# Optimization experiments

Measured on AMD Instinct MI355X. Metric: run time of the kernel, lower is better.

## Reference

```python
import jax, jax.numpy as jnp
import numpy as np

N = 16777216  # batch*A*width*height (flat anchor-score vector)
BINS = 10
LOSS_WEIGHT = 1.0


def setup_inputs() -> dict:
    key = jax.random.key(0)
    k1, k2, k3 = jax.random.split(key, 3)
    pred = jax.random.normal(k1, (N,), dtype=jnp.float32)          # IoU logits
    target = jax.random.uniform(k2, (N,), dtype=jnp.float32)       # IoU targets in [0,1]
    label_weight = (jax.random.uniform(k3, (N,)) > 0.3).astype(jnp.float32)  # 1=valid, 0=ignore
    return {"pred": pred, "target": target, "label_weight": label_weight, "bins": BINS}


def reference(pred, target, label_weight, bins):
    # target is detached in the original module
    target = jax.lax.stop_gradient(target)
    # gradient norm g = |sigmoid(pred).detach() - target|, lies in [0,1]
    g = jnp.abs(jax.lax.stop_gradient(jax.nn.sigmoid(pred)) - target)
    valid = label_weight > 0
    validf = valid.astype(jnp.float32)
    tot = jnp.maximum(jnp.sum(validf), 1.0)

    # edges are i/bins with last edge nudged by 1e-6, so bin = floor(g*bins) clipped to bins-1
    bin_idx = jnp.clip((g * bins).astype(jnp.int32), 0, bins - 1)
    counts = jax.ops.segment_sum(validf, bin_idx, num_segments=bins)  # per-bin valid counts
    n = jnp.sum(counts > 0).astype(jnp.float32)                        # number of nonempty bins
    counts_safe = jnp.maximum(counts, 1.0)
    w_per_bin = jnp.where(counts > 0, tot / counts_safe, 0.0) / jnp.maximum(n, 1.0)
    weights = jnp.where(valid, w_per_bin[bin_idx], 0.0)

    # weighted BCE-with-logits, reduction='sum', stable form: logaddexp(0,x) - x*z
    bce = jnp.logaddexp(0.0, pred) - pred * target
    loss = jnp.sum(weights * bce) / tot
    return loss * LOSS_WEIGHT
```

## Files before the change

### kernel.cpp

```cpp
#include <hip/hip_runtime.h>

#define BINS 10
#define REPLICAS 16
#define NBLOCKS 2048
#define NTHREADS 256


typedef float vfloat4 __attribute__((ext_vector_type(4)));

__global__ __launch_bounds__(NTHREADS, 4)
void ghm_pass1(const float* __restrict__ pred,
               const float* __restrict__ target,
               const float* __restrict__ lw,
               float* __restrict__ rep_sums,
               unsigned int* __restrict__ rep_cnts,
               int n)
{
    __shared__ float ls[BINS];
    __shared__ unsigned int lc[BINS];
    if (threadIdx.x < BINS) { ls[threadIdx.x] = 0.0f; lc[threadIdx.x] = 0u; }

    float s0=0.f,s1=0.f,s2=0.f,s3=0.f,s4=0.f,s5=0.f,s6=0.f,s7=0.f,s8=0.f,s9=0.f;
    unsigned long long cpk = 0ull;

#define SBIN(B, S) { (S) += (bi_ == (B)) ? bce_ : 0.0f; }
#define PROC(P, T, W) do {                                                     \
    float p_ = (P), t_ = (T);                                                  \
    float ap_ = fabsf(p_);                                                     \
    float q_  = __builtin_amdgcn_exp2f(ap_ * -1.4426950408889634f); \
    float r_  = __builtin_amdgcn_rcpf(1.0f + q_);                              \
    float sig_ = (p_ >= 0.0f) ? r_ : (1.0f - r_);                              \
    float g_   = fabsf(sig_ - t_);                                             \
    int bi_ = (int)(g_ * 10.0f);                                               \
    bi_ = bi_ > 9 ? 9 : bi_;                                                   \
    bi_ = ((W) > 0.0f) ? bi_ : 10;              \
    float bce_ = fmaxf(p_, 0.0f)                                               \
               + 0.6931471805599453f * __builtin_amdgcn_logf(1.0f + q_)        \
               - p_ * t_;                                                      \
    cpk += 1ull << (6 * bi_);                                                  \
    SBIN(0,s0) SBIN(1,s1) SBIN(2,s2) SBIN(3,s3) SBIN(4,s4)                     \
    SBIN(5,s5) SBIN(6,s6) SBIN(7,s7) SBIN(8,s8) SBIN(9,s9)                     \
} while (0)
#define PROC4(PV, TV, WV) {                                                    \
    PROC((PV).x, (TV).x, (WV).x);                                              \
    PROC((PV).y, (TV).y, (WV).y);                                              \
    PROC((PV).z, (TV).z, (WV).z);                                              \
    PROC((PV).w, (TV).w, (WV).w); }

    const int n4 = n >> 2;
    const int full = n4 / (NBLOCKS * NTHREADS);
    const vfloat4* p4 = (const vfloat4*)pred;
    const vfloat4* t4 = (const vfloat4*)target;
    const vfloat4* w4 = (const vfloat4*)lw;

    if (full == 8) {
        const int base = blockIdx.x * 8 * NTHREADS + threadIdx.x;
        vfloat4 P[8], T[8], W[8];
        #pragma unroll
        for (int j = 0; j < 8; ++j) {
            P[j] = __builtin_nontemporal_load(&p4[base + j * NTHREADS]);
            T[j] = __builtin_nontemporal_load(&t4[base + j * NTHREADS]);
            W[j] = __builtin_nontemporal_load(&w4[base + j * NTHREADS]);
        }
        #pragma unroll
        for (int j = 0; j < 8; ++j) {
            PROC4(P[j], T[j], W[j]);
        }
    } else if (full >= 2) {
        const int base = blockIdx.x * full * NTHREADS + threadIdx.x;
        vfloat4 pA = p4[base], tA = t4[base], wA = w4[base];
        vfloat4 pB = p4[base + NTHREADS], tB = t4[base + NTHREADS],
                wB = w4[base + NTHREADS];
        for (int j = 2; j < full; ++j) {
            const int idx = base + j * NTHREADS;
            vfloat4 pC = p4[idx], tC = t4[idx], wC = w4[idx];
            PROC4(pA, tA, wA);
            pA = pB; tA = tB; wA = wB;
            pB = pC; tB = tC; wB = wC;
        }
        PROC4(pA, tA, wA);
        PROC4(pB, tB, wB);
    }
    const int gid = blockIdx.x * NTHREADS + threadIdx.x;
    const int stride = NBLOCKS * NTHREADS;
    for (int i = full * stride + gid; i < n4; i += stride) {
        vfloat4 pv = p4[i], tv = t4[i], wv = w4[i];
        PROC4(pv, tv, wv);
    }
    for (int j = (n4 << 2) + gid; j < n; j += stride) {
        PROC(pred[j], target[j], lw[j]);
    }

    unsigned int c0 = (unsigned int)(cpk       ) & 63u;
    unsigned int c1 = (unsigned int)(cpk >>  6 ) & 63u;
    unsigned int c2 = (unsigned int)(cpk >> 12 ) & 63u;
    unsigned int c3 = (unsigned int)(cpk >> 18 ) & 63u;
    unsigned int c4 = (unsigned int)(cpk >> 24 ) & 63u;
    unsigned int c5 = (unsigned int)(cpk >> 30 ) & 63u;
    unsigned int c6 = (unsigned int)(cpk >> 36 ) & 63u;
    unsigned int c7 = (unsigned int)(cpk >> 42 ) & 63u;
    unsigned int c8 = (unsigned int)(cpk >> 48 ) & 63u;
    unsigned int c9 = (unsigned int)(cpk >> 54 ) & 63u;

#define WREDUCE(S, C) {                                                        \
    _Pragma("unroll")                                                          \
    for (int o_ = 32; o_ > 0; o_ >>= 1) {                                      \
        (S) += __shfl_down((S), o_, 64);                                       \
        (C) += __shfl_down((C), o_, 64);                                       \
    } }
    WREDUCE(s0,c0) WREDUCE(s1,c1) WREDUCE(s2,c2) WREDUCE(s3,c3) WREDUCE(s4,c4)
    WREDUCE(s5,c5) WREDUCE(s6,c6) WREDUCE(s7,c7) WREDUCE(s8,c8) WREDUCE(s9,c9)

    __syncthreads();
    if ((threadIdx.x & 63) == 0) {
        atomicAdd(&ls[0], s0); atomicAdd(&lc[0], c0);
        atomicAdd(&ls[1], s1); atomicAdd(&lc[1], c1);
        atomicAdd(&ls[2], s2); atomicAdd(&lc[2], c2);
        atomicAdd(&ls[3], s3); atomicAdd(&lc[3], c3);
        atomicAdd(&ls[4], s4); atomicAdd(&lc[4], c4);
        atomicAdd(&ls[5], s5); atomicAdd(&lc[5], c5);
        atomicAdd(&ls[6], s6); atomicAdd(&lc[6], c6);
        atomicAdd(&ls[7], s7); atomicAdd(&lc[7], c7);
        atomicAdd(&ls[8], s8); atomicAdd(&lc[8], c8);
        atomicAdd(&ls[9], s9); atomicAdd(&lc[9], c9);
    }
    __syncthreads();
    if (threadIdx.x < BINS) {
        int rep = blockIdx.x & (REPLICAS - 1);
        atomicAdd(&rep_sums[rep * BINS + threadIdx.x], ls[threadIdx.x]);
        atomicAdd(&rep_cnts[rep * BINS + threadIdx.x], lc[threadIdx.x]);
    }
#undef PROC
#undef PROC4
#undef SBIN
#undef WREDUCE
}

__global__ void ghm_finalize(const float* __restrict__ rep_sums,
                             const unsigned int* __restrict__ rep_cnts,
                             float* __restrict__ out)
{
    __shared__ double S[BINS];
    __shared__ unsigned int C[BINS];
    int t = threadIdx.x;
    if (t < BINS) {
        double s = 0.0;
        unsigned int cc = 0u;
        for (int r = 0; r < REPLICAS; ++r) {
            s += (double)rep_sums[r * BINS + t];
            cc += rep_cnts[r * BINS + t];
        }
        S[t] = s;
        C[t] = cc;
    }
    __syncthreads();
    if (t == 0) {
        double n_ne = 0.0;
        for (int b = 0; b < BINS; ++b) if (C[b] > 0u) n_ne += 1.0;
        double nn = n_ne > 1.0 ? n_ne : 1.0;
        double loss = 0.0;
        for (int b = 0; b < BINS; ++b)
            if (C[b] > 0u) loss += S[b] / ((double)C[b] * nn);
        out[0] = (float)loss;
    }
}

extern "C" void kernel_launch(void* const* d_in, const int* in_sizes, int n_in,
                              void* d_out, int out_size, void* d_ws, size_t ws_size,
                              hipStream_t stream)
{
    const float* pred = (const float*)d_in[0];
    const float* target = (const float*)d_in[1];
    const float* lw = (const float*)d_in[2];
    int n = in_sizes[0];

    float* rep_sums = (float*)d_ws;
    unsigned int* rep_cnts =
        (unsigned int*)((char*)d_ws + REPLICAS * BINS * sizeof(float));

    (void)hipMemsetAsync(d_ws, 0, 2 * REPLICAS * BINS * sizeof(float), stream);
    ghm_pass1<<<NBLOCKS, NTHREADS, 0, stream>>>(pred, target, lw,
                                                rep_sums, rep_cnts, n);
    ghm_finalize<<<1, 64, 0, stream>>>(rep_sums, rep_cnts, (float*)d_out);
}
```

Before: 203.3 us.

## Stream main-path inputs through LDS via async global_load_lds ring buffer

In the full==8 path, the upfront register-held nontemporal loads are replaced with global_load_lds transfers. These write directly into a per-wave 4-slot LDS ring, and explicit s_waitcnt vmcnt steps overlap the loads with computation. The aim is to cut VGPR pressure and keep several loads in flight while earlier tiles are processed. The cost is 48 KB of static LDS per block, which can lower the number of resident blocks per CU, plus an extra LDS read per element.

```diff
diff --git a/kernel.cpp b/kernel.cpp
--- a/kernel.cpp
+++ b/kernel.cpp
@@ -7,6 +7,12 @@
 
 
 typedef float vfloat4 __attribute__((ext_vector_type(4)));
+
+#define AS1 __attribute__((address_space(1)))
+#define AS3 __attribute__((address_space(3)))
+#define GLL(gp, lp) __builtin_amdgcn_global_load_lds(                          \
+    (const AS1 void*)(gp), (AS3 void*)(lp), 16, 0, 0)
+#define VMW(N) asm volatile("s_waitcnt vmcnt(" #N ")" ::: "memory")
 
 __global__ __launch_bounds__(NTHREADS, 4)
 void ghm_pass1(const float* __restrict__ pred,
@@ -16,6 +22,7 @@
                unsigned int* __restrict__ rep_cnts,
                int n)
 {
+    __shared__ vfloat4 stage[4 * 4 * 3 * 64];
     __shared__ float ls[BINS];
     __shared__ unsigned int lc[BINS];
     if (threadIdx.x < BINS) { ls[threadIdx.x] = 0.0f; lc[threadIdx.x] = 0u; }
@@ -55,17 +62,36 @@
 
     if (full == 8) {
         const int base = blockIdx.x * 8 * NTHREADS + threadIdx.x;
-        vfloat4 P[8], T[8], W[8];
-        #pragma unroll
-        for (int j = 0; j < 8; ++j) {
-            P[j] = __builtin_nontemporal_load(&p4[base + j * NTHREADS]);
-            T[j] = __builtin_nontemporal_load(&t4[base + j * NTHREADS]);
-            W[j] = __builtin_nontemporal_load(&w4[base + j * NTHREADS]);
-        }
-        #pragma unroll
-        for (int j = 0; j < 8; ++j) {
-            PROC4(P[j], T[j], W[j]);
-        }
+        const int lane = threadIdx.x & 63;
+        vfloat4* stw = &stage[(threadIdx.x >> 6) * 768];
+
+#define ISSUE(T) do {                                                          \
+        const int g_ = base + (T) * NTHREADS;                                  \
+        vfloat4* d_ = &stw[((T) & 3) * 192];                                   \
+        GLL(&p4[g_], d_);                                                      \
+        GLL(&t4[g_], d_ + 64);                                                 \
+        GLL(&w4[g_], d_ + 128);                                                \
+    } while (0)
+#define STEP(T, VMLIT) do {                                                    \
+        VMW(VMLIT);                                                            \
+        const vfloat4* r_ = &stw[((T) & 3) * 192 + lane];                      \
+        vfloat4 pv = r_[0];                                                    \
+        vfloat4 tv = r_[64];                                                   \
+        vfloat4 wv = r_[128];                                                  \
+        PROC4(pv, tv, wv);                                                     \
+    } while (0)
+
+        ISSUE(0); ISSUE(1); ISSUE(2);
+        ISSUE(3); STEP(0, 9);
+        ISSUE(4); STEP(1, 9);
+        ISSUE(5); STEP(2, 9);
+        ISSUE(6); STEP(3, 9);
+        ISSUE(7); STEP(4, 9);
+        STEP(5, 6);
+        STEP(6, 3);
+        STEP(7, 0);
+#undef ISSUE
+#undef STEP
     } else if (full >= 2) {
         const int base = blockIdx.x * full * NTHREADS + threadIdx.x;
         vfloat4 pA = p4[base], tA = t4[base], wA = w4[base];
```

Result: no change. 204.5 us (+0.6%).
